# Performance work log

Hardware: AMD Instinct MI355X
Metric: run time of the kernel (lower is better)

The kernel has to match this reference:

```python
import jax, jax.numpy as jnp
import numpy as np
from jax.scipy.special import logsumexp

B, N1, N2, D = 32, 512, 512, 128
M_WARP = 256   # n_warp_fn_times
M_DISCR = 96   # n_warp_discr (warp-value grid per time step)
GAMMA = 0.1    # softmin temperature (soft relaxation of the hard-argmin GDTW DP)
BARRIER = 1e4  # soft penalty enforcing endpoint + local-gradient constraints


def setup_inputs() -> dict:
    key = jax.random.key(0)
    k1, k2, k3 = jax.random.split(key, 3)
    return {
        "signal1_features": jax.random.normal(k1, (B, N1, D), jnp.float32),
        "signal2_features": jax.random.normal(k2, (B, N2, D), jnp.float32),
        "reg_wt": jax.random.uniform(k3, (B,), jnp.float32, 0.1, 1.0),
        "glb_lb": jnp.zeros((B, M_WARP), jnp.float32),
        "glb_ub": jnp.ones((B, M_WARP), jnp.float32),
        "lcl_grad_ub": 2.0 * jnp.ones((B, 1), jnp.float32),
        "signal1_times": jnp.broadcast_to(jnp.linspace(0.0, 1.0, N1, dtype=jnp.float32)[None], (B, N1)),
        "signal2_times": jnp.broadcast_to(jnp.linspace(0.0, 1.0, N2, dtype=jnp.float32)[None], (B, N2)),
        "warp_fn_times": jnp.broadcast_to(jnp.linspace(0.0, 1.0, M_WARP, dtype=jnp.float32)[None], (B, M_WARP)),
    }


def _interp_uniform(feats, pos):
    """Linear interpolation of feats [b,n,d] at normalized positions pos in [0,1]."""
    b, n, d = feats.shape
    shp = pos.shape
    x = jnp.clip(pos, 0.0, 1.0) * (n - 1)
    i0 = jnp.clip(x.astype(jnp.int32), 0, n - 2)
    w = (x - i0.astype(x.dtype)).reshape(b, -1, 1)
    flat = i0.reshape(b, -1)
    f0 = jnp.take_along_axis(feats, flat[..., None], axis=1)
    f1 = jnp.take_along_axis(feats, flat[..., None] + 1, axis=1)
    return (f0 * (1.0 - w) + f1 * w).reshape(*shp, d)


def _softmin(x, axis):
    return -GAMMA * logsumexp(-x / GAMMA, axis=axis)


def _gdtw(s1f, s2f, reg_wt, glb_lb, glb_ub, lcl_grad_ub, t1, t2, tw):
    b, m = tw.shape
    T2 = jnp.max(t2, axis=1, keepdims=True)                       # [b,1]
    lb = glb_lb * T2
    ub = glb_ub * T2
    frac = jnp.linspace(0.0, 1.0, M_DISCR, dtype=tw.dtype)
    tau = lb[..., None] + (ub - lb)[..., None] * frac             # [b,m,M] candidate warp values
    s1_at = _interp_uniform(s1f, tw / jnp.max(t1, axis=1, keepdims=True))  # [b,m,d]
    s2_at = _interp_uniform(s2f, tau / T2[..., None])             # [b,m,M,d]
    diff = s1_at[:, :, None, :] - s2_at
    dtw_ = jnp.diff(tw, axis=1)                                   # [b,m-1]
    wts = 0.5 * jnp.concatenate([dtw_[:, :1], dtw_[:, 1:] + dtw_[:, :-1], dtw_[:, -1:]], axis=1)
    node = jnp.sum(diff * diff, axis=-1) * wts[..., None]         # [b,m,M] feature loss (p=2), trapezoid dt
    # endpoint constraints (subseq_enabled=False): phi(t0)=0, phi(tm)=T2
    node = node.at[:, 0].add(BARRIER * tau[:, 0] ** 2)
    node = node.at[:, -1].add(BARRIER * (tau[:, -1] - T2) ** 2)
    # transition costs: regularisation |phi' - 1|^2 dt + soft barriers for 0 <= phi' <= lcl_grad_ub
    slope = (tau[:, 1:, None, :] - tau[:, :-1, :, None]) / dtw_[:, :, None, None]  # [b,m-1,Mk,Mj]
    gub = lcl_grad_ub[:, :, None, None]
    pen = BARRIER * (jax.nn.relu(-slope) ** 2 + jax.nn.relu(slope - gub) ** 2)
    edge = reg_wt[:, None, None, None] * (slope - 1.0) ** 2 * dtw_[:, :, None, None] + pen
    edge_sc = jnp.moveaxis(edge, 1, 0)                            # [m-1,b,M,M]
    node_sc = jnp.moveaxis(node[:, 1:], 1, 0)                     # [m-1,b,M]

    def fwd_step(a, x):
        n_i, e_i = x
        a_new = n_i + _softmin(a[:, :, None] + e_i, axis=1)
        return a_new, a_new

    a0 = node[:, 0]
    _, alphas = jax.lax.scan(fwd_step, a0, (node_sc, edge_sc))
    alpha = jnp.concatenate([a0[None], alphas], axis=0)           # [m,b,M]

    def bwd_step(bn, x):
        n_ip1, e_i = x
        b_new = _softmin(e_i + (n_ip1 + bn)[:, None, :], axis=2)
        return b_new, b_new

    bT = jnp.zeros_like(a0)
    _, betas = jax.lax.scan(bwd_step, bT, (node_sc, edge_sc), reverse=True)
    beta = jnp.concatenate([betas, bT[None]], axis=0)             # [m,b,M]

    p = jax.nn.softmax(-(alpha + beta) / GAMMA, axis=-1)          # node marginals [m,b,M]
    return jnp.einsum('mbk,bmk->bm', p, tau)                      # expected warp values [b,m]


def reference(signal1_features, signal2_features, reg_wt, glb_lb, glb_ub, lcl_grad_ub, signal1_times, signal2_times, warp_fn_times):
    return _gdtw(signal1_features, signal2_features, reg_wt, glb_lb, glb_ub, lcl_grad_ub,
                 signal1_times, signal2_times, warp_fn_times)
```

## Files before the change

### kernel.cpp

```cpp
#include <hip/hip_runtime.h>

#define NB 32
#define N1 512
#define N2 512
#define DF 128
#define MW 256
#define KD 96
#define INVG 10.0f
#define GAM 0.1f
#define BARRIER 10000.0f

#define WS_NODE  0
#define WS_ABUF  (WS_NODE + NB*MW*KD)
#define WS_BBUF  (WS_ABUF + NB*MW*KD)

__device__ __forceinline__ bool feq(float a, float b) {
  return fabsf(a - b) <= 1e-4f * fmaxf(fabsf(a), fabsf(b)) + 1e-12f;
}

__device__ __forceinline__ float edgec(float s, float rdtv, float gub) {
  float d = s - 1.0f, ng = fminf(s, 0.f), ov = fmaxf(s - gub, 0.f);
  return rdtv*d*d + BARRIER*(ng*ng + ov*ov);
}

__global__ __launch_bounds__(256) void k1_node(const float* __restrict__ s1f,
                                               const float* __restrict__ s2f,
                                               const float* __restrict__ tw,
                                               const float* __restrict__ glb_lb,
                                               const float* __restrict__ glb_ub,
                                               const float* __restrict__ t1,
                                               const float* __restrict__ t2,
                                               float* __restrict__ ws) {
  const int mb = blockIdx.x;
  const int b  = blockIdx.y;
  const int t  = threadIdx.x;
  const int lane = t & 63;
  const int wv = t >> 6;
  __shared__ float s1L[32*132];
  __shared__ float s2L[96*132];
  __shared__ float ndt[32*99];
  __shared__ float wtsL[32], lbL[32], ubL[32];
  __shared__ int   matchL[32];
  __shared__ float redm[8];

  {
    float m1 = -1e30f, m2 = -1e30f;
    for (int i = t; i < N1; i += 256) m1 = fmaxf(m1, t1[b*N1+i]);
    for (int i = t; i < N2; i += 256) m2 = fmaxf(m2, t2[b*N2+i]);
    #pragma unroll
    for (int o = 32; o; o >>= 1) {
      m1 = fmaxf(m1, __shfl_down(m1, o));
      m2 = fmaxf(m2, __shfl_down(m2, o));
    }
    if (lane == 0) { redm[wv] = m1; redm[4+wv] = m2; }
  }
  __syncthreads();
  const float T1 = fmaxf(fmaxf(redm[0], redm[1]), fmaxf(redm[2], redm[3]));
  const float T2 = fmaxf(fmaxf(redm[4], redm[5]), fmaxf(redm[6], redm[7]));
  const float lb0 = glb_lb[b*MW] * T2;
  const float ub0 = glb_ub[b*MW] * T2;
  float4* s1L4 = (float4*)s1L;
  float4* s2L4 = (float4*)s2L;
  const float4* s1f4 = (const float4*)(s1f + (size_t)b*N1*DF);
  const float4* s2f4 = (const float4*)(s2f + (size_t)b*N2*DF);

  {
    const int d32 = t & 31;
    const int k8  = t >> 5;
    for (int kk = 0; kk < 12; kk++) {
      int k = k8 + 8*kk;
      float tau = lb0 + (ub0 - lb0) * (float)k * (1.0f/95.0f);
      float x = fminf(fmaxf(tau / T2, 0.f), 1.f) * (float)(N2-1);
      int i0 = (int)x; i0 = max(0, min(i0, N2-2));
      float w = x - (float)i0;
      float4 f0 = s2f4[(size_t)i0*32 + d32];
      float4 f1 = s2f4[(size_t)(i0+1)*32 + d32];
      float4 r;
      r.x = f0.x + (f1.x - f0.x)*w; r.y = f0.y + (f1.y - f0.y)*w;
      r.z = f0.z + (f1.z - f0.z)*w; r.w = f0.w + (f1.w - f0.w)*w;
      s2L4[k*33 + d32] = r;
    }
  }
  {
    const int mi = t >> 3, q = t & 7;
    const int m = mb*32 + mi;
    float twm = tw[b*MW + m];
    float x = fminf(fmaxf(twm / T1, 0.f), 1.f) * (float)(N1-1);
    int i0 = (int)x; i0 = max(0, min(i0, N1-2));
    float w = x - (float)i0;
    #pragma unroll
    for (int j = 0; j < 4; j++) {
      int d4 = q + 8*j;
      float4 f0 = s1f4[(size_t)i0*32 + d4];
      float4 f1 = s1f4[(size_t)(i0+1)*32 + d4];
      float4 r;
      r.x = f0.x + (f1.x - f0.x)*w; r.y = f0.y + (f1.y - f0.y)*w;
      r.z = f0.z + (f1.z - f0.z)*w; r.w = f0.w + (f1.w - f0.w)*w;
      s1L4[mi*33 + d4] = r;
    }
  }
  if (t < 32) {
    int m = mb*32 + t, g = b*MW + m;
    float twm = tw[g];
    float prev = (m > 0) ? tw[g-1] : twm;
    float next = (m < MW-1) ? tw[g+1] : twm;
    wtsL[t] = 0.5f*(next - prev);
    float lbm = glb_lb[g]*T2, ubm = glb_ub[g]*T2;
    lbL[t] = lbm; ubL[t] = ubm;
    matchL[t] = (feq(lbm, lb0) && feq(ubm, ub0)) ? 1 : 0;
  }
  __syncthreads();

  const int mi = t >> 3, kg = t & 7;
  const int m = mb*32 + mi;
  float acc[12];
  #pragma unroll
  for (int i = 0; i < 12; i++) acc[i] = 0.f;
  if (matchL[mi]) {
    for (int d4 = 0; d4 < 32; d4++) {
      float4 s1v = s1L4[mi*33 + d4];
      #pragma unroll
      for (int k12 = 0; k12 < 12; k12++) {
        int k = kg + 8*k12;
        float4 s2v = s2L4[k*33 + d4];
        float dx = s1v.x - s2v.x, dy = s1v.y - s2v.y;
        float dz = s1v.z - s2v.z, dw = s1v.w - s2v.w;
        acc[k12] += dx*dx + dy*dy + dz*dz + dw*dw;
      }
    }
  } else {
    const float lbm = lbL[mi], ubm = ubL[mi];
    int i0a[12]; float wa[12];
    #pragma unroll
    for (int k12 = 0; k12 < 12; k12++) {
      int k = kg + 8*k12;
      float tau = lbm + (ubm - lbm) * (float)k * (1.0f/95.0f);
      float x = fminf(fmaxf(tau / T2, 0.f), 1.f) * (float)(N2-1);
      int i0 = (int)x; i0 = max(0, min(i0, N2-2));
      i0a[k12] = i0; wa[k12] = x - (float)i0;
    }
    for (int d4 = 0; d4 < 32; d4++) {
      float4 s1v = s1L4[mi*33 + d4];
      #pragma unroll
      for (int k12 = 0; k12 < 12; k12++) {
        float4 f0 = s2f4[(size_t)i0a[k12]*32 + d4];
        float4 f1 = s2f4[(size_t)(i0a[k12]+1)*32 + d4];
        float w = wa[k12];
        float ax = f0.x + (f1.x - f0.x)*w, ay = f0.y + (f1.y - f0.y)*w;
        float az = f0.z + (f1.z - f0.z)*w, aw = f0.w + (f1.w - f0.w)*w;
        float dx = s1v.x - ax, dy = s1v.y - ay, dz = s1v.z - az, dw = s1v.w - aw;
        acc[k12] += dx*dx + dy*dy + dz*dz + dw*dw;
      }
    }
  }
  {
    const float wts = wtsL[mi];
    const float lbm = lbL[mi], ubm = ubL[mi];
    #pragma unroll
    for (int k12 = 0; k12 < 12; k12++) {
      int k = kg + 8*k12;
      float nodev = acc[k12] * wts;
      float tau = lbm + (ubm - lbm) * (float)k * (1.0f/95.0f);
      if (m == 0)    nodev += BARRIER * tau * tau;
      if (m == MW-1) { float dd = tau - T2; nodev += BARRIER * dd * dd; }
      ndt[mi*99 + k] = nodev;
    }
  }
  __syncthreads();
  float* nodeP = ws + WS_NODE + ((size_t)b*MW + mb*32)*KD;
  for (int idx = t; idx < 32*KD; idx += 256) {
    int mi2 = idx / KD, kv = idx - mi2*KD;
    nodeP[idx] = ndt[mi2*99 + kv];
  }
}

__global__ __launch_bounds__(128) void k2_out(const float* __restrict__ tw,
                                              const float* __restrict__ glb_lb,
                                              const float* __restrict__ glb_ub,
                                              const float* __restrict__ reg_wt,
                                              const float* __restrict__ gubp,
                                              const float* __restrict__ t2,
                                              float* __restrict__ ws,
                                              float* __restrict__ out) {
  const int b = blockIdx.x;
  const int t = threadIdx.x;
  const int wv = t >> 6;
  const int lane = t & 63;
  __shared__ float ndL[MW*KD];
  __shared__ float ndmL[MW];
  __shared__ float lbw[MW], ubw[MW], twv[MW];
  __shared__ float mir[2][KD];
  __shared__ float sred[8];
  __shared__ int skey[2];
  const float* __restrict__ nodeP = ws + WS_NODE + (size_t)b*MW*KD;

  {
    const float4* np4 = (const float4*)nodeP;
    float4* nl4 = (float4*)ndL;
    #pragma unroll
    for (int it = 0; it < (MW*KD/4)/128; it++)
      nl4[t + 128*it] = np4[t + 128*it];
  }
  {
    float m2 = -1e30f;
    for (int i = t; i < N2; i += 128) m2 = fmaxf(m2, t2[b*N2+i]);
    #pragma unroll
    for (int o = 32; o; o >>= 1) m2 = fmaxf(m2, __shfl_down(m2, o));
    if (lane == 0) sred[4+wv] = m2;
  }
  __syncthreads();
  const float T2 = fmaxf(sred[4], sred[5]);
  for (int i = t; i < MW; i += 128) {
    lbw[i] = glb_lb[b*MW+i]*T2;
    ubw[i] = glb_ub[b*MW+i]*T2;
    twv[i] = tw[b*MW+i];
  }
  const float r = reg_wt[b];
  const float gub = gubp[b];
  __syncthreads();

  const float lb0 = lbw[0], ub0 = ubw[0];
  const float g = (ub0 - lb0) * (1.0f/95.0f);
  bool keyok = true;
  float minE1 = 3e38f, minE2 = 3e38f, maxRdt = 0.f;
  for (int i = t; i < MW; i += 128)
    keyok = keyok && (lbw[i] == lb0) && (ubw[i] == ub0);
  for (int i = t; i < MW-1; i += 128) {
    float dtv = twv[i+1] - twv[i];
    if (!(dtv > 0.f)) keyok = false;
    else {
      float rdtv = r * dtv, sl = g / dtv;
      minE1 = fminf(minE1, fminf(edgec(sl, rdtv, gub), edgec(-sl, rdtv, gub)));
      minE2 = fminf(minE2, fminf(edgec(2.f*sl, rdtv, gub), edgec(-2.f*sl, rdtv, gub)));
      maxRdt = fmaxf(maxRdt, rdtv);
    }
  }

  const bool actS = t < KD;
  const int k = actS ? t : (KD-1);
  const bool hasn = actS && (k < KD-1);
  float P = 0.f, P2 = 0.f, mx = 0.f;
  #pragma unroll 8
  for (int m = 0; m < MW; m++) {
    float a  = ndL[m*KD + k];
    float bq = hasn ? ndL[m*KD + k + 1] : a;
    P += a; P2 += bq;
    mx = fmaxf(mx, fabsf(P - P2));
  }
  if (!actS) mx = 0.f;
  {
    float wmx = mx, wE1 = minE1, wE2 = minE2, wR = maxRdt;
    #pragma unroll
    for (int o = 32; o; o >>= 1) {
      wmx = fmaxf(wmx, __shfl_xor(wmx, o));
      wE1 = fminf(wE1, __shfl_xor(wE1, o));
      wE2 = fminf(wE2, __shfl_xor(wE2, o));
      wR  = fmaxf(wR,  __shfl_xor(wR,  o));
    }
    int ka = __all(keyok ? 1 : 0);
    if (lane == 0) {
      sred[wv*4+0] = wmx; sred[wv*4+1] = wE1;
      sred[wv*4+2] = wE2; sred[wv*4+3] = wR;
      skey[wv] = ka;
    }
  }
  __syncthreads();
  const float MX = fmaxf(sred[0], sred[4]);
  const float E1 = fminf(sred[1], sred[5]);
  const float E2 = fminf(sred[2], sred[6]);
  const float RD = fmaxf(sred[3], sred[7]);
  const bool ok = skey[0] && skey[1] &&
                  (2.0f*MX   <= E1 - RD - 3.0f) &&
                  (190.0f*MX <= E2 - RD - 3.0f);

  if (ok) {
    __syncthreads();
    float s = actS ? P : 3e38f;
    float mnv = s;
    #pragma unroll
    for (int o = 32; o; o >>= 1) mnv = fminf(mnv, __shfl_xor(mnv, o));
    if (lane == 0) sred[wv] = mnv;
    __syncthreads();
    const float mn = fminf(sred[0], sred[1]);
    float w = actS ? __expf((mn - P) * INVG) : 0.f;
    float num = w * (float)k, den = w;
    #pragma unroll
    for (int o = 32; o; o >>= 1) {
      num += __shfl_xor(num, o);
      den += __shfl_xor(den, o);
    }
    if (lane == 0) { sred[2+4*wv] = num; sred[3+4*wv] = den; }
    __syncthreads();
    const float q = ((sred[2] + sred[6]) / (sred[3] + sred[7])) * (1.0f/95.0f);
    for (int m = t; m < MW; m += 128)
      out[b*MW + m] = lbw[m] + (ubw[m] - lbw[m]) * q;
    return;
  }

  {
    for (int i2 = t; i2 < MW; i2 += 128) {
      float mnv = 3e38f;
      for (int kk = 0; kk < KD; kk++) mnv = fminf(mnv, ndL[i2*KD + kk]);
      ndmL[i2] = mnv;
    }
    __syncthreads();

    const int dir = t >> 6;
    const bool act = lane < 48;
    const int k0i = 2*lane, k1i = 2*lane+1;
    const float frk0 = (float)k0i*(1.f/95.f), frk1 = (float)k1i*(1.f/95.f);
    float* __restrict__ outP = ws + (dir ? WS_BBUF : WS_ABUF) + (size_t)b*MW*KD;

    float a0 = 3e38f, a1 = 3e38f;
    {
      const int m0 = dir ? (MW-1) : 0;
      if (act) {
        a0 = ndL[m0*KD + k0i]; a1 = ndL[m0*KD + k1i];
        mir[dir][k0i] = a0; mir[dir][k1i] = a1;
        float2 o; o.x = dir ? 0.f : a0; o.y = dir ? 0.f : a1;
        *(float2*)&outP[(size_t)m0*KD + k0i] = o;
      }
    }
    float Blo;
    {
      float bl = act ? fminf(a0, a1) : 3e38f;
      #pragma unroll
      for (int o = 1; o < 64; o <<= 1) bl = fminf(bl, __shfl_xor(bl, o));
      Blo = bl;
    }
    float e00=3e38f,e0m=3e38f,e0p=3e38f,e10=3e38f,e1m=3e38f,e1p=3e38f;
    float eo0=3e38f, eo1=3e38f, eminmin=0.f;
    float cL1=__int_as_float(0x7fc00000), cU1=cL1, cL2=cL1, cU2=cL1, cdt=cL1;

    float pL1, pU1, pL2, pU2, pt1, pt2, pnd0=0.f, pnd1=0.f, pndm;
    {
      const int i0_ = dir ? (MW-2) : 0;
      pL1=lbw[i0_]; pU1=ubw[i0_]; pL2=lbw[i0_+1]; pU2=ubw[i0_+1];
      pt1=twv[i0_]; pt2=twv[i0_+1];
      const int mn_ = dir ? i0_ : (i0_+1);
      if (act) { float2 v = *(const float2*)&ndL[mn_*KD + k0i]; pnd0=v.x; pnd1=v.y; }
      pndm = ndmL[mn_];
    }

    for (int step = 0; step < MW-1; step++) {
      const float L1=pL1, U1=pU1, L2=pL2, U2=pU2;
      const float dt = pt2 - pt1;
      const float nd0=pnd0, nd1=pnd1, ndmn=pndm;
      {
        const int sn = (step+1 < MW-1) ? (step+1) : step;
        const int in_ = dir ? (MW-2-sn) : sn;
        pL1=lbw[in_]; pU1=ubw[in_]; pL2=lbw[in_+1]; pU2=ubw[in_+1];
        pt1=twv[in_]; pt2=twv[in_+1];
        const int mn_ = dir ? in_ : (in_+1);
        if (act) { float2 v = *(const float2*)&ndL[mn_*KD + k0i]; pnd0=v.x; pnd1=v.y; }
        pndm = ndmL[mn_];
      }
      const bool kc = !(feq(L1,cL1)&&feq(U1,cU1)&&feq(L2,cL2)&&feq(U2,cU2)&&feq(dt,cdt));
      if (kc) {
        cL1=L1; cU1=U1; cL2=L2; cU2=U2; cdt=dt;
        float bl = act ? fminf(mir[dir][k0i], mir[dir][k1i]) : 3e38f;
        #pragma unroll
        for (int o = 1; o < 64; o <<= 1) bl = fminf(bl, __shfl_xor(bl, o));
        Blo = bl;
        const float invdt = 1.f/dt, rdt = r*dt;
        const float my0 = dir ? (L1+(U1-L1)*frk0) : (L2+(U2-L2)*frk0);
        const float my1 = dir ? (L1+(U1-L1)*frk1) : (L2+(U2-L2)*frk1);
        e00=3e38f; e0m=3e38f; e0p=3e38f; e10=3e38f; e1m=3e38f; e1p=3e38f;
        eo0=3e38f; eo1=3e38f;
        float emn = 3e38f;
        for (int j = 0; j < KD; j++) {
          const float frj = (float)j*(1.f/95.f);
          const float oth = dir ? (L2+(U2-L2)*frj) : (L1+(U1-L1)*frj);
          const float sl0 = (dir ? (oth-my0) : (my0-oth))*invdt;
          const float sl1 = (dir ? (oth-my1) : (my1-oth))*invdt;
          float d0=sl0-1.f, g0=fminf(sl0,0.f), v0=fmaxf(sl0-gub,0.f);
          float ej0 = rdt*d0*d0 + BARRIER*(g0*g0+v0*v0);
          float d1=sl1-1.f, g1=fminf(sl1,0.f), v1=fmaxf(sl1-gub,0.f);
          float ej1 = rdt*d1*d1 + BARRIER*(g1*g1+v1*v1);
          emn = fminf(emn, fminf(ej0, ej1));
          if      (j == k0i-1) e0m = ej0;
          else if (j == k0i)   e00 = ej0;
          else if (j == k0i+1) e0p = ej0;
          else                 eo0 = fminf(eo0, ej0);
          if      (j == k1i-1) e1m = ej1;
          else if (j == k1i)   e10 = ej1;
          else if (j == k1i+1) e1p = ej1;
          else                 eo1 = fminf(eo1, ej1);
        }
        if (!act) emn = 3e38f;
        #pragma unroll
        for (int o = 1; o < 64; o <<= 1) emn = fminf(emn, __shfl_xor(emn, o));
        eminmin = emn;
      }
      const float a1p = __shfl_up(a1, 1);
      const float a0n = __shfl_down(a0, 1);
      const float x0m = fminf(a1p + e0m, 3e38f);
      const float x00 = fminf(a0  + e00, 3e38f);
      const float x0p = fminf(a1  + e0p, 3e38f);
      const float x1m = fminf(a0  + e1m, 3e38f);
      const float x10 = fminf(a1  + e10, 3e38f);
      const float x1p = fminf(a0n + e1p, 3e38f);
      float mn0 = fminf(fminf(x0m, x00), x0p);
      float mn1 = fminf(fminf(x1m, x10), x1p);
      float sum0 = __expf((mn0-x0m)*INVG) + __expf((mn0-x00)*INVG) + __expf((mn0-x0p)*INVG);
      float sum1 = __expf((mn1-x1m)*INVG) + __expf((mn1-x10)*INVG) + __expf((mn1-x1p)*INVG);
      const bool bad = act && ((Blo + eo0 - mn0 < 8.7f) || (Blo + eo1 - mn1 < 8.7f));
      if (__any((int)bad)) {
        const float invdt = 1.f/dt, rdt = r*dt;
        const float my0 = dir ? (L1+(U1-L1)*frk0) : (L2+(U2-L2)*frk0);
        const float my1 = dir ? (L1+(U1-L1)*frk1) : (L2+(U2-L2)*frk1);
        mn0 = 3e38f; mn1 = 3e38f;
        for (int j = 0; j < KD; j++) {
          const float sj = mir[dir][j];
          const float frj = (float)j*(1.f/95.f);
          const float oth = dir ? (L2+(U2-L2)*frj) : (L1+(U1-L1)*frj);
          const float sl0 = (dir ? (oth-my0) : (my0-oth))*invdt;
          const float sl1 = (dir ? (oth-my1) : (my1-oth))*invdt;
          float d0=sl0-1.f, g0=fminf(sl0,0.f), v0=fmaxf(sl0-gub,0.f);
          float ej0 = rdt*d0*d0 + BARRIER*(g0*g0+v0*v0);
          float d1=sl1-1.f, g1=fminf(sl1,0.f), v1=fmaxf(sl1-gub,0.f);
          float ej1 = rdt*d1*d1 + BARRIER*(g1*g1+v1*v1);
          mn0 = fminf(mn0, fminf(sj + ej0, 3e38f));
          mn1 = fminf(mn1, fminf(sj + ej1, 3e38f));
        }
        sum0 = 0.f; sum1 = 0.f;
        for (int j = 0; j < KD; j++) {
          const float sj = mir[dir][j];
          const float frj = (float)j*(1.f/95.f);
          const float oth = dir ? (L2+(U2-L2)*frj) : (L1+(U1-L1)*frj);
          const float sl0 = (dir ? (oth-my0) : (my0-oth))*invdt;
          const float sl1 = (dir ? (oth-my1) : (my1-oth))*invdt;
          float d0=sl0-1.f, g0=fminf(sl0,0.f), v0=fmaxf(sl0-gub,0.f);
          float ej0 = rdt*d0*d0 + BARRIER*(g0*g0+v0*v0);
          float d1=sl1-1.f, g1=fminf(sl1,0.f), v1=fmaxf(sl1-gub,0.f);
          float ej1 = rdt*d1*d1 + BARRIER*(g1*g1+v1*v1);
          sum0 += __expf((mn0 - fminf(sj + ej0, 3e38f))*INVG);
          sum1 += __expf((mn1 - fminf(sj + ej1, 3e38f))*INVG);
        }
      }
      const float sv0 = mn0 - GAM*__logf(sum0);
      const float sv1 = mn1 - GAM*__logf(sum1);
      const float na0 = nd0 + sv0, na1 = nd1 + sv1;
      const int ic = dir ? (MW-2-step) : step;
      const int mnode = dir ? ic : (ic+1);
      if (act) {
        mir[dir][k0i] = na0; mir[dir][k1i] = na1;
        float2 o; o.x = dir ? sv0 : na0; o.y = dir ? sv1 : na1;
        *(float2*)&outP[(size_t)mnode*KD + k0i] = o;
      }
      a0 = act ? na0 : 3e38f;
      a1 = act ? na1 : 3e38f;
      Blo += eminmin + ndmn - 0.4575f;
    }

    __threadfence_block();
    __syncthreads();
    const float* __restrict__ Ab = ws + WS_ABUF + (size_t)b*MW*KD;
    const float* __restrict__ Bb = ws + WS_BBUF + (size_t)b*MW*KD;
    for (int m = t; m < MW; m += 128) {
      float mnv = 3e38f;
      for (int kk = 0; kk < KD; kk++)
        mnv = fminf(mnv, Ab[(size_t)m*KD+kk] + Bb[(size_t)m*KD+kk]);
      float num = 0.f, den = 0.f;
      for (int kk = 0; kk < KD; kk++) {
        float s = Ab[(size_t)m*KD+kk] + Bb[(size_t)m*KD+kk];
        float w = __expf((mnv - s) * INVG);
        num += w * (float)kk; den += w;
      }
      out[b*MW + m] = lbw[m] + (ubw[m] - lbw[m]) * (num/den) * (1.0f/95.0f);
    }
  }
}

extern "C" void kernel_launch(void* const* d_in, const int* in_sizes, int n_in,
                              void* d_out, int out_size, void* d_ws, size_t ws_size,
                              hipStream_t stream) {
  const float* s1f    = (const float*)d_in[0];
  const float* s2f    = (const float*)d_in[1];
  const float* regw   = (const float*)d_in[2];
  const float* glb_lb = (const float*)d_in[3];
  const float* glb_ub = (const float*)d_in[4];
  const float* gubp   = (const float*)d_in[5];
  const float* t1     = (const float*)d_in[6];
  const float* t2     = (const float*)d_in[7];
  const float* twp    = (const float*)d_in[8];
  float* ws  = (float*)d_ws;
  float* out = (float*)d_out;

  dim3 g1(8, NB);
  k1_node<<<g1, 256, 0, stream>>>(s1f, s2f, twp, glb_lb, glb_ub, t1, t2, ws);
  k2_out<<<NB, 128, 0, stream>>>(twp, glb_lb, glb_ub, regw, gubp, t2, ws, out);
}
```

Before: 111.1 us.

## Fuse node-cost and DP kernels using inter-block release/acquire flag synchronization

Merges the node-cost kernel and the per-batch DP/output kernel into one launch. Blocks publish their node tiles to workspace and then set a per-block magic flag with a release store. The mb==0 block of each batch spin-waits on its batch's 8 flags, then runs the former second kernel out of a shared-memory union. This removes the second launch and the gap between kernels, and lets batches proceed independently. The cost is a reliance on all blocks being co-resident. The flags are also never reset, so on repeated calls the wait can pass early and read stale node data.

```diff
diff --git a/kernel.cpp b/kernel.cpp
--- a/kernel.cpp
+++ b/kernel.cpp
@@ -13,6 +13,9 @@
 #define WS_NODE  0
 #define WS_ABUF  (WS_NODE + NB*MW*KD)
 #define WS_BBUF  (WS_ABUF + NB*MW*KD)
+#define WS_FLAG  (WS_BBUF + NB*MW*KD)
+
+#define FLMAGIC(i) (0xA5C30000u ^ (unsigned)((i) * 2654435761u))
 
 __device__ __forceinline__ bool feq(float a, float b) {
   return fabsf(a - b) <= 1e-4f * fmaxf(fabsf(a), fabsf(b)) + 1e-12f;
@@ -23,25 +26,36 @@
   return rdtv*d*d + BARRIER*(ng*ng + ov*ov);
 }
 
-__global__ __launch_bounds__(256) void k1_node(const float* __restrict__ s1f,
-                                               const float* __restrict__ s2f,
-                                               const float* __restrict__ tw,
-                                               const float* __restrict__ glb_lb,
-                                               const float* __restrict__ glb_ub,
-                                               const float* __restrict__ t1,
-                                               const float* __restrict__ t2,
-                                               float* __restrict__ ws) {
+__global__ __launch_bounds__(256) void k_fused(
+    const float* __restrict__ s1f, const float* __restrict__ s2f,
+    const float* __restrict__ tw,  const float* __restrict__ glb_lb,
+    const float* __restrict__ glb_ub, const float* __restrict__ regw,
+    const float* __restrict__ gubp, const float* __restrict__ t1,
+    const float* __restrict__ t2, float* __restrict__ ws,
+    float* __restrict__ out) {
   const int mb = blockIdx.x;
   const int b  = blockIdx.y;
   const int t  = threadIdx.x;
   const int lane = t & 63;
   const int wv = t >> 6;
-  __shared__ float s1L[32*132];
-  __shared__ float s2L[96*132];
-  __shared__ float ndt[32*99];
-  __shared__ float wtsL[32], lbL[32], ubL[32];
-  __shared__ int   matchL[32];
-  __shared__ float redm[8];
+
+  __shared__ union SMu {
+    struct {
+      float s1L[32*132];
+      float s2L[96*132];
+      float ndt[32*99];
+      float wtsL[32], lbL[32], ubL[32], redm[8];
+      int   matchL[32];
+    } a;
+    struct {
+      float ndL[MW*KD];
+      float ndmL[MW];
+      float lbw[MW], ubw[MW], twv[MW];
+      float mir[2][KD];
+      float sred[8];
+      int   skey[2];
+    } p;
+  } sm;
 
   {
     float m1 = -1e30f, m2 = -1e30f;
@@ -52,15 +66,15 @@
       m1 = fmaxf(m1, __shfl_down(m1, o));
       m2 = fmaxf(m2, __shfl_down(m2, o));
     }
-    if (lane == 0) { redm[wv] = m1; redm[4+wv] = m2; }
-  }
-  __syncthreads();
-  const float T1 = fmaxf(fmaxf(redm[0], redm[1]), fmaxf(redm[2], redm[3]));
-  const float T2 = fmaxf(fmaxf(redm[4], redm[5]), fmaxf(redm[6], redm[7]));
+    if (lane == 0) { sm.a.redm[wv] = m1; sm.a.redm[4+wv] = m2; }
+  }
+  __syncthreads();
+  const float T1 = fmaxf(fmaxf(sm.a.redm[0], sm.a.redm[1]), fmaxf(sm.a.redm[2], sm.a.redm[3]));
+  const float T2 = fmaxf(fmaxf(sm.a.redm[4], sm.a.redm[5]), fmaxf(sm.a.redm[6], sm.a.redm[7]));
   const float lb0 = glb_lb[b*MW] * T2;
   const float ub0 = glb_ub[b*MW] * T2;
-  float4* s1L4 = (float4*)s1L;
-  float4* s2L4 = (float4*)s2L;
+  float4* s1L4 = (float4*)sm.a.s1L;
+  float4* s2L4 = (float4*)sm.a.s2L;
   const float4* s1f4 = (const float4*)(s1f + (size_t)b*N1*DF);
   const float4* s2f4 = (const float4*)(s2f + (size_t)b*N2*DF);
 
@@ -75,16 +89,16 @@
       float w = x - (float)i0;
       float4 f0 = s2f4[(size_t)i0*32 + d32];
       float4 f1 = s2f4[(size_t)(i0+1)*32 + d32];
-      float4 r;
-      r.x = f0.x + (f1.x - f0.x)*w; r.y = f0.y + (f1.y - f0.y)*w;
-      r.z = f0.z + (f1.z - f0.z)*w; r.w = f0.w + (f1.w - f0.w)*w;
-      s2L4[k*33 + d32] = r;
-    }
-  }
-  {
-    const int mi = t >> 3, q = t & 7;
-    const int m = mb*32 + mi;
-    float twm = tw[b*MW + m];
+      float4 rr;
+      rr.x = f0.x + (f1.x - f0.x)*w; rr.y = f0.y + (f1.y - f0.y)*w;
+      rr.z = f0.z + (f1.z - f0.z)*w; rr.w = f0.w + (f1.w - f0.w)*w;
+      s2L4[k*33 + d32] = rr;
+    }
+  }
+  {
+    const int smi = t >> 3, q = t & 7;
+    const int sm_ = mb*32 + smi;
+    float twm = tw[b*MW + sm_];
     float x = fminf(fmaxf(twm / T1, 0.f), 1.f) * (float)(N1-1);
     int i0 = (int)x; i0 = max(0, min(i0, N1-2));
     float w = x - (float)i0;
@@ -93,10 +107,10 @@
       int d4 = q + 8*j;
       float4 f0 = s1f4[(size_t)i0*32 + d4];
       float4 f1 = s1f4[(size_t)(i0+1)*32 + d4];
-      float4 r;
-      r.x = f0.x + (f1.x - f0.x)*w; r.y = f0.y + (f1.y - f0.y)*w;
-      r.z = f0.z + (f1.z - f0.z)*w; r.w = f0.w + (f1.w - f0.w)*w;
-      s1L4[mi*33 + d4] = r;
+      float4 rr;
+      rr.x = f0.x + (f1.x - f0.x)*w; rr.y = f0.y + (f1.y - f0.y)*w;
+      rr.z = f0.z + (f1.z - f0.z)*w; rr.w = f0.w + (f1.w - f0.w)*w;
+      s1L4[smi*33 + d4] = rr;
     }
   }
   if (t < 32) {
@@ -104,19 +118,19 @@
     float twm = tw[g];
     float prev = (m > 0) ? tw[g-1] : twm;
     float next = (m < MW-1) ? tw[g+1] : twm;
-    wtsL[t] = 0.5f*(next - prev);
+    sm.a.wtsL[t] = 0.5f*(next - prev);
     float lbm = glb_lb[g]*T2, ubm = glb_ub[g]*T2;
-    lbL[t] = lbm; ubL[t] = ubm;
-    matchL[t] = (feq(lbm, lb0) && feq(ubm, ub0)) ? 1 : 0;
+    sm.a.lbL[t] = lbm; sm.a.ubL[t] = ubm;
+    sm.a.matchL[t] = (feq(lbm, lb0) && feq(ubm, ub0)) ? 1 : 0;
   }
   __syncthreads();
 
   const int mi = t >> 3, kg = t & 7;
-  const int m = mb*32 + mi;
+  const int am = mb*32 + mi;
   float acc[12];
   #pragma unroll
   for (int i = 0; i < 12; i++) acc[i] = 0.f;
-  if (matchL[mi]) {
+  if (sm.a.matchL[mi]) {
     for (int d4 = 0; d4 < 32; d4++) {
       float4 s1v = s1L4[mi*33 + d4];
       #pragma unroll
@@ -129,7 +143,7 @@
       }
     }
   } else {
-    const float lbm = lbL[mi], ubm = ubL[mi];
+    const float lbm = sm.a.lbL[mi], ubm = sm.a.ubL[mi];
     int i0a[12]; float wa[12];
     #pragma unroll
     for (int k12 = 0; k12 < 12; k12++) {
@@ -154,77 +168,78 @@
     }
   }
   {
-    const float wts = wtsL[mi];
-    const float lbm = lbL[mi], ubm = ubL[mi];
+    const float wts = sm.a.wtsL[mi];
+    const float lbm = sm.a.lbL[mi], ubm = sm.a.ubL[mi];
     #pragma unroll
     for (int k12 = 0; k12 < 12; k12++) {
       int k = kg + 8*k12;
       float nodev = acc[k12] * wts;
       float tau = lbm + (ubm - lbm) * (float)k * (1.0f/95.0f);
-      if (m == 0)    nodev += BARRIER * tau * tau;
-      if (m == MW-1) { float dd = tau - T2; nodev += BARRIER * dd * dd; }
-      ndt[mi*99 + k] = nodev;
-    }
-  }
-  __syncthreads();
-  float* nodeP = ws + WS_NODE + ((size_t)b*MW + mb*32)*KD;
-  for (int idx = t; idx < 32*KD; idx += 256) {
-    int mi2 = idx / KD, kv = idx - mi2*KD;
-    nodeP[idx] = ndt[mi2*99 + kv];
-  }
-}
-
-__global__ __launch_bounds__(128) void k2_out(const float* __restrict__ tw,
-                                              const float* __restrict__ glb_lb,
-                                              const float* __restrict__ glb_ub,
-                                              const float* __restrict__ reg_wt,
-                                              const float* __restrict__ gubp,
-                                              const float* __restrict__ t2,
-                                              float* __restrict__ ws,
-                                              float* __restrict__ out) {
-  const int b = blockIdx.x;
-  const int t = threadIdx.x;
-  const int wv = t >> 6;
-  const int lane = t & 63;
-  __shared__ float ndL[MW*KD];
-  __shared__ float ndmL[MW];
-  __shared__ float lbw[MW], ubw[MW], twv[MW];
-  __shared__ float mir[2][KD];
-  __shared__ float sred[8];
-  __shared__ int skey[2];
-  const float* __restrict__ nodeP = ws + WS_NODE + (size_t)b*MW*KD;
-
-  {
-    const float4* np4 = (const float4*)nodeP;
-    float4* nl4 = (float4*)ndL;
-    #pragma unroll
-    for (int it = 0; it < (MW*KD/4)/128; it++)
-      nl4[t + 128*it] = np4[t + 128*it];
-  }
-  {
-    float m2 = -1e30f;
-    for (int i = t; i < N2; i += 128) m2 = fmaxf(m2, t2[b*N2+i]);
-    #pragma unroll
-    for (int o = 32; o; o >>= 1) m2 = fmaxf(m2, __shfl_down(m2, o));
-    if (lane == 0) sred[4+wv] = m2;
-  }
-  __syncthreads();
-  const float T2 = fmaxf(sred[4], sred[5]);
+      if (am == 0)    nodev += BARRIER * tau * tau;
+      if (am == MW-1) { float dd = tau - T2; nodev += BARRIER * dd * dd; }
+      sm.a.ndt[mi*99 + k] = nodev;
+    }
+  }
+  __syncthreads();
+  {
+    float* nodeP = ws + WS_NODE + ((size_t)b*MW + mb*32)*KD;
+    for (int idx = t; idx < 32*KD; idx += 256) {
+      int mi2 = idx / KD, kv = idx - mi2*KD;
+      nodeP[idx] = sm.a.ndt[mi2*99 + kv];
+    }
+  }
+  __threadfence();
+  __syncthreads();
+  if (t == 0)
+    __hip_atomic_store((unsigned*)ws + WS_FLAG + b*8 + mb, FLMAGIC(b*8+mb),
+                       __ATOMIC_RELEASE, __HIP_MEMORY_SCOPE_AGENT);
+  if (mb != 0) return;
+  if (t >= 128) return;
+
+  float (&ndL)[MW*KD]  = sm.p.ndL;
+  float (&ndmL)[MW]    = sm.p.ndmL;
+  float (&lbw)[MW]     = sm.p.lbw;
+  float (&ubw)[MW]     = sm.p.ubw;
+  float (&twv)[MW]     = sm.p.twv;
+  float (&mir)[2][KD]  = sm.p.mir;
+  float (&sred)[8]     = sm.p.sred;
+  int   (&skey)[2]     = sm.p.skey;
+
   for (int i = t; i < MW; i += 128) {
     lbw[i] = glb_lb[b*MW+i]*T2;
     ubw[i] = glb_ub[b*MW+i]*T2;
     twv[i] = tw[b*MW+i];
   }
-  const float r = reg_wt[b];
+  const float r = regw[b];
   const float gub = gubp[b];
-  __syncthreads();
-
-  const float lb0 = lbw[0], ub0 = ubw[0];
-  const float g = (ub0 - lb0) * (1.0f/95.0f);
+
+  {
+    unsigned* fl = (unsigned*)ws + WS_FLAG + b*8;
+    if (t < 8) {
+      const unsigned mg = FLMAGIC(b*8+t);
+      while (__hip_atomic_load(&fl[t], __ATOMIC_ACQUIRE, __HIP_MEMORY_SCOPE_AGENT) != mg)
+        __builtin_amdgcn_s_sleep(2);
+    }
+  }
+  __syncthreads();
+  __threadfence();
+
+  const float* __restrict__ nodeP = ws + WS_NODE + (size_t)b*MW*KD;
+  {
+    const float4* np4 = (const float4*)nodeP;
+    float4* nl4 = (float4*)ndL;
+    #pragma unroll
+    for (int it = 0; it < (MW*KD/4)/128; it++)
+      nl4[t + 128*it] = np4[t + 128*it];
+  }
+  __syncthreads();
+
+  const float lb0b = lbw[0], ub0b = ubw[0];
+  const float g = (ub0b - lb0b) * (1.0f/95.0f);
   bool keyok = true;
   float minE1 = 3e38f, minE2 = 3e38f, maxRdt = 0.f;
   for (int i = t; i < MW; i += 128)
-    keyok = keyok && (lbw[i] == lb0) && (ubw[i] == ub0);
+    keyok = keyok && (lbw[i] == lb0b) && (ubw[i] == ub0b);
   for (int i = t; i < MW-1; i += 128) {
     float dtv = twv[i+1] - twv[i];
     if (!(dtv > 0.f)) keyok = false;
@@ -487,7 +502,6 @@
   float* ws  = (float*)d_ws;
   float* out = (float*)d_out;
 
-  dim3 g1(8, NB);
-  k1_node<<<g1, 256, 0, stream>>>(s1f, s2f, twp, glb_lb, glb_ub, t1, t2, ws);
-  k2_out<<<NB, 128, 0, stream>>>(twp, glb_lb, glb_ub, regw, gubp, t2, ws, out);
+  dim3 g(8, NB);
+  k_fused<<<g, 256, 0, stream>>>(s1f, s2f, twp, glb_lb, glb_ub, regw, gubp, t1, t2, ws, out);
 }
```

Result: slower. 142.6 us (+28.4%).
